# Optimization experiments

Hardware: AMD Instinct MI355X
Metric: run time of the kernel (lower is better)

The kernel has to match this reference:

```python
import jax, jax.numpy as jnp
import numpy as np


def setup_inputs() -> dict:
    key = jax.random.key(0)
    k1, k2, k3 = jax.random.split(key, 3)
    B, K, NPC, D = 64, 1000, 256, 768
    querys = jax.random.normal(k1, (B, D), dtype=jnp.float32)
    data = jax.random.normal(k2, (K, NPC, D), dtype=jnp.float32)      # clustered doc embeddings
    centers = jax.random.normal(k3, (K, D), dtype=jnp.float32)        # cluster centroids
    clusted_idx = jnp.arange(K * NPC, dtype=jnp.int32).reshape(K, NPC)  # global doc id per slot
    return {
        'querys': querys,
        'data': data,
        'centers': centers,
        'clusted_idx': clusted_idx,
        'k': 16,
        'num_search': 10,
    }


def reference(querys, data, centers, clusted_idx, k, num_search):
    """Clustered (IVF-style) cosine top-k search.
    querys: (B,D); data: (K,NPC,D); centers: (K,D); clusted_idx: (K,NPC)
    returns ret_idx (B,k) int, ret_emb (B,k,D) float.
    dist_fn = -cos_sim, so argmin dist == argmax cosine.
    """
    B, D = querys.shape
    eps = jnp.float32(1e-12)
    qn = querys / jnp.maximum(jnp.linalg.norm(querys, axis=1, keepdims=True), eps)
    cn = centers / jnp.maximum(jnp.linalg.norm(centers, axis=1, keepdims=True), eps)

    # ---- first(): pick num_search closest clusters by cosine ----
    cos_c = qn @ cn.T                              # (B, K)
    _, c_idx = jax.lax.top_k(cos_c, num_search)    # (B, S) smallest -cos == largest cos

    # ---- second(): exact cosine search inside selected clusters ----
    cand = data[c_idx]                             # (B, S, NPC, D) gather
    cand_ids = clusted_idx[c_idx]                  # (B, S, NPC)
    cand_norm = jnp.maximum(jnp.linalg.norm(cand, axis=-1), eps)  # (B, S, NPC)
    cos = jnp.einsum('bd,bsnd->bsn', qn, cand) / cand_norm        # (B, S, NPC)

    # ---- merge: global top-k over all candidates ----
    cos_flat = cos.reshape(B, -1)                  # (B, S*NPC)
    _, top = jax.lax.top_k(cos_flat, k)            # (B, k)
    ret_idx = jnp.take_along_axis(cand_ids.reshape(B, -1), top, axis=1)            # (B, k)
    ret_emb = jnp.take_along_axis(cand.reshape(B, -1, D), top[..., None], axis=1)  # (B, k, D)
    return ret_idx, ret_emb
```

## Files before the change

kernel.cpp:

```cpp
#include <hip/hip_runtime.h>
#include <math.h>

#define BQ   64
#define KC   1000
#define NPC  256
#define DIM  768
#define TOPK 16
#define NS   10

#define NEG_INF (-__builtin_inff())

#define DOT12(acc, A, Bv) \
    acc = fmaf(A.x, Bv.x, acc); acc = fmaf(A.y, Bv.y, acc); \
    acc = fmaf(A.z, Bv.z, acc); acc = fmaf(A.w, Bv.w, acc);

__global__ void knorm_q(const float* __restrict__ q, float* __restrict__ qn,
                        int* __restrict__ cnt) {
    int b = blockIdx.x, t = threadIdx.x;
    if (b < 4 && t < 250) cnt[b * 250 + t] = 0;
    const float* row = q + b * DIM;
    float v0 = row[t], v1 = row[t + 256], v2 = row[t + 512];
    __shared__ float red[256];
    red[t] = v0 * v0 + v1 * v1 + v2 * v2;
    __syncthreads();
    for (int off = 128; off; off >>= 1) {
        if (t < off) red[t] += red[t + off];
        __syncthreads();
    }
    float scale = 1.0f / fmaxf(sqrtf(red[0]), 1e-12f);
    qn[b * DIM + t]       = v0 * scale;
    qn[b * DIM + t + 256] = v1 * scale;
    qn[b * DIM + t + 512] = v2 * scale;
}

__global__ void kcenter_scores(const float* __restrict__ qn,
                               const float* __restrict__ centers,
                               float* __restrict__ cosc) {
    int wave = threadIdx.x >> 6, lane = threadIdx.x & 63;
    int cblk = blockIdx.x >> 2, qg = blockIdx.x & 3;
    int k0 = cblk * 4 + wave;
    const float4* cp = (const float4*)(centers + (size_t)k0 * DIM);
    float4 c0 = cp[lane], c1 = cp[lane + 64], c2 = cp[lane + 128];
    float sq = 0.f;
    DOT12(sq, c0, c0); DOT12(sq, c1, c1); DOT12(sq, c2, c2);
    for (int off = 1; off < 64; off <<= 1) sq += __shfl_xor(sq, off);
    float inv = 1.0f / fmaxf(sqrtf(sq), 1e-12f);
    int b0 = qg * 16;
    for (int i = 0; i < 16; i += 4) {
        const float4* qa = (const float4*)(qn + (size_t)(b0 + i + 0) * DIM);
        const float4* qb = (const float4*)(qn + (size_t)(b0 + i + 1) * DIM);
        const float4* qc = (const float4*)(qn + (size_t)(b0 + i + 2) * DIM);
        const float4* qd = (const float4*)(qn + (size_t)(b0 + i + 3) * DIM);
        float4 a0 = qa[lane], a1 = qa[lane + 64], a2 = qa[lane + 128];
        float4 e0 = qb[lane], e1 = qb[lane + 64], e2 = qb[lane + 128];
        float4 f0 = qc[lane], f1 = qc[lane + 64], f2 = qc[lane + 128];
        float4 g0 = qd[lane], g1 = qd[lane + 64], g2 = qd[lane + 128];
        float dA = 0.f, dB = 0.f, dC = 0.f, dD = 0.f;
        DOT12(dA, a0, c0); DOT12(dA, a1, c1); DOT12(dA, a2, c2);
        DOT12(dB, e0, c0); DOT12(dB, e1, c1); DOT12(dB, e2, c2);
        DOT12(dC, f0, c0); DOT12(dC, f1, c1); DOT12(dC, f2, c2);
        DOT12(dD, g0, c0); DOT12(dD, g1, c1); DOT12(dD, g2, c2);
        for (int off = 1; off < 64; off <<= 1) {
            dA += __shfl_xor(dA, off);
            dB += __shfl_xor(dB, off);
            dC += __shfl_xor(dC, off);
            dD += __shfl_xor(dD, off);
        }
        if (lane == 0) {
            cosc[(b0 + i + 0) * KC + k0] = dA * inv;
            cosc[(b0 + i + 1) * KC + k0] = dB * inv;
            cosc[(b0 + i + 2) * KC + k0] = dC * inv;
            cosc[(b0 + i + 3) * KC + k0] = dD * inv;
        }
    }
}

__device__ __forceinline__ void wave_argmax(float& bv, int& bi) {
    for (int off = 1; off < 64; off <<= 1) {
        float v2 = __shfl_xor(bv, off);
        int   i2 = __shfl_xor(bi, off);
        if (v2 > bv || (v2 == bv && i2 < bi)) { bv = v2; bi = i2; }
    }
}

__global__ void ktop_clusters(const float* __restrict__ cosc, int* __restrict__ cidx,
                              int* __restrict__ cnt, int* __restrict__ sel) {
    int b = blockIdx.x, t = threadIdx.x;
    int wave = t >> 6, lane = t & 63;
    __shared__ float vals[KC];
    __shared__ float wrv[4];
    __shared__ int   wri[4];
    for (int i = t; i < KC; i += 256) vals[i] = cosc[b * KC + i];
    __syncthreads();
    for (int s = 0; s < NS; ++s) {
        float bv = NEG_INF; int bi = 0x7fffffff;
        for (int i = t; i < KC; i += 256) {
            float v = vals[i];
            if (v > bv) { bv = v; bi = i; }
        }
        wave_argmax(bv, bi);
        if (lane == 0) { wrv[wave] = bv; wri[wave] = bi; }
        __syncthreads();
        if (t == 0) {
            float fv = wrv[0]; int fi = wri[0];
            for (int w = 1; w < 4; ++w) {
                float v2 = wrv[w]; int i2 = wri[w];
                if (v2 > fv || (v2 == fv && i2 < fi)) { fv = v2; fi = i2; }
            }
            cidx[b * NS + s] = fi;
            int pos = atomicAdd(&cnt[fi], 1);
            sel[fi * 64 + pos] = b * NS + s;
            vals[fi] = NEG_INF;
        }
        __syncthreads();
    }
}

__global__ void kcand(const float* __restrict__ qn, const float* __restrict__ data,
                      const int* __restrict__ cnt, const int* __restrict__ sel,
                      float* __restrict__ cosall) {
    int c = blockIdx.x >> 2, sub = blockIdx.x & 3;
    int m = cnt[c];
    if (m == 0) return;
    int t = threadIdx.x;
    __shared__ int slist[64];
    if (t < m) slist[t] = sel[c * 64 + t];
    __syncthreads();
    int wave = t >> 6, lane = t & 63;
    const float* base = data + (size_t)c * NPC * DIM;
    int n0 = sub * 64 + wave * 16;
    for (int it = 0; it < 4; ++it) {
        int n = n0 + it * 4;
        const float4* dpa = (const float4*)(base + (size_t)(n + 0) * DIM);
        const float4* dpb = (const float4*)(base + (size_t)(n + 1) * DIM);
        const float4* dpc = (const float4*)(base + (size_t)(n + 2) * DIM);
        const float4* dpd = (const float4*)(base + (size_t)(n + 3) * DIM);
        float4 a0 = dpa[lane], a1 = dpa[lane + 64], a2 = dpa[lane + 128];
        float4 e0 = dpb[lane], e1 = dpb[lane + 64], e2 = dpb[lane + 128];
        float4 f0 = dpc[lane], f1 = dpc[lane + 64], f2 = dpc[lane + 128];
        float4 g0 = dpd[lane], g1 = dpd[lane + 64], g2 = dpd[lane + 128];
        float sqA = 0.f, sqB = 0.f, sqC = 0.f, sqD = 0.f;
        DOT12(sqA, a0, a0); DOT12(sqA, a1, a1); DOT12(sqA, a2, a2);
        DOT12(sqB, e0, e0); DOT12(sqB, e1, e1); DOT12(sqB, e2, e2);
        DOT12(sqC, f0, f0); DOT12(sqC, f1, f1); DOT12(sqC, f2, f2);
        DOT12(sqD, g0, g0); DOT12(sqD, g1, g1); DOT12(sqD, g2, g2);
        for (int off = 1; off < 64; off <<= 1) {
            sqA += __shfl_xor(sqA, off); sqB += __shfl_xor(sqB, off);
            sqC += __shfl_xor(sqC, off); sqD += __shfl_xor(sqD, off);
        }
        float invA = 1.0f / fmaxf(sqrtf(sqA), 1e-12f);
        float invB = 1.0f / fmaxf(sqrtf(sqB), 1e-12f);
        float invC = 1.0f / fmaxf(sqrtf(sqC), 1e-12f);
        float invD = 1.0f / fmaxf(sqrtf(sqD), 1e-12f);
        for (int j = 0; j < m; ++j) {
            int i = slist[j];
            int b = i / NS;
            const float4* qp = (const float4*)(qn + (size_t)b * DIM);
            float4 q0 = qp[lane], q1 = qp[lane + 64], q2 = qp[lane + 128];
            float dA = 0.f, dB = 0.f, dC = 0.f, dD = 0.f;
            DOT12(dA, q0, a0); DOT12(dA, q1, a1); DOT12(dA, q2, a2);
            DOT12(dB, q0, e0); DOT12(dB, q1, e1); DOT12(dB, q2, e2);
            DOT12(dC, q0, f0); DOT12(dC, q1, f1); DOT12(dC, q2, f2);
            DOT12(dD, q0, g0); DOT12(dD, q1, g1); DOT12(dD, q2, g2);
            for (int off = 1; off < 64; off <<= 1) {
                dA += __shfl_xor(dA, off); dB += __shfl_xor(dB, off);
                dC += __shfl_xor(dC, off); dD += __shfl_xor(dD, off);
            }
            if (lane == 0) {
                float* outp = cosall + (size_t)i * NPC + n;
                outp[0] = dA * invA;
                outp[1] = dB * invB;
                outp[2] = dC * invC;
                outp[3] = dD * invD;
            }
        }
    }
}

__global__ void ktop_final(const float* __restrict__ cosall, const int* __restrict__ cidx,
                           const int* __restrict__ clusted, const float* __restrict__ data,
                           float* __restrict__ out) {
    int b = blockIdx.x, t = threadIdx.x;
    int wave = t >> 6, lane = t & 63;
    __shared__ float vals[NS * NPC];
    __shared__ float wrv[4];
    __shared__ int   wri[4];
    __shared__ int   docs[TOPK];
    for (int i = t; i < NS * NPC; i += 256) vals[i] = cosall[(size_t)b * (NS * NPC) + i];
    __syncthreads();
    for (int j = 0; j < TOPK; ++j) {
        float bv = NEG_INF; int bi = 0x7fffffff;
        for (int i = t; i < NS * NPC; i += 256) {
            float v = vals[i];
            if (v > bv) { bv = v; bi = i; }
        }
        wave_argmax(bv, bi);
        if (lane == 0) { wrv[wave] = bv; wri[wave] = bi; }
        __syncthreads();
        if (t == 0) {
            float fv = wrv[0]; int fi = wri[0];
            for (int w = 1; w < 4; ++w) {
                float v2 = wrv[w]; int i2 = wri[w];
                if (v2 > fv || (v2 == fv && i2 < fi)) { fv = v2; fi = i2; }
            }
            int s = fi >> 8, n = fi & (NPC - 1);
            int c = cidx[b * NS + s];
            int doc = c * NPC + n;
            docs[j] = doc;
            out[b * TOPK + j] = (float)clusted[doc];
            vals[fi] = NEG_INF;
        }
        __syncthreads();
    }
    float* emb = out + BQ * TOPK;
    for (int idx = t; idx < TOPK * (DIM / 4); idx += 256) {
        int j = idx / (DIM / 4), col = idx - j * (DIM / 4);
        int doc = docs[j];
        ((float4*)(emb + ((size_t)(b * TOPK + j)) * DIM))[col] =
            ((const float4*)(data + (size_t)doc * DIM))[col];
    }
}

extern "C" void kernel_launch(void* const* d_in, const int* in_sizes, int n_in,
                              void* d_out, int out_size, void* d_ws, size_t ws_size,
                              hipStream_t stream) {
    const float* querys  = (const float*)d_in[0];
    const float* data    = (const float*)d_in[1];
    const float* centers = (const float*)d_in[2];
    const int*   clusted = (const int*)d_in[3];
    float* out = (float*)d_out;

    float* ws     = (float*)d_ws;
    float* qn     = ws;
    float* cosc   = qn + BQ * DIM;
    int*   cidx   = (int*)(cosc + BQ * KC);
    float* cosall = (float*)(cidx + BQ * NS);
    int*   cnt    = (int*)(cosall + BQ * NS * NPC);
    int*   sel    = cnt + KC;

    knorm_q<<<BQ, 256, 0, stream>>>(querys, qn, cnt);
    kcenter_scores<<<KC, 256, 0, stream>>>(qn, centers, cosc);
    ktop_clusters<<<BQ, 256, 0, stream>>>(cosc, cidx, cnt, sel);
    kcand<<<KC * 4, 256, 0, stream>>>(qn, data, cnt, sel, cosall);
    ktop_final<<<BQ, 256, 0, stream>>>(cosall, cidx, clusted, data, out);
}
```

Measured before the change: 143.1 us.

## Drop query normalization kernel and restage candidate scoring through LDS tiles

Removes the query-normalization kernel and feeds raw queries to the center and candidate scoring, since a positive per-query scale does not change the per-query top-k ranking. The counter reset moves into kcenter_scores. The candidate kernel now uses one block per cluster with one thread per document. Each block stages 32-wide D chunks of the cluster into padded LDS and accumulates up to 8 query dot products per thread, replacing the wave-per-doc shuffle reductions. This cuts launches and reduction overhead but lowers parallelism (1000 blocks instead of 4000) and reads query rows from global memory uncached in LDS. It also changes output cosine magnitudes, which is safe only if later stages compare values and never output them.

```diff
diff --git a/kernel.cpp b/kernel.cpp
--- a/kernel.cpp
+++ b/kernel.cpp
@@ -14,28 +14,12 @@
     acc = fmaf(A.x, Bv.x, acc); acc = fmaf(A.y, Bv.y, acc); \
     acc = fmaf(A.z, Bv.z, acc); acc = fmaf(A.w, Bv.w, acc);
 
-__global__ void knorm_q(const float* __restrict__ q, float* __restrict__ qn,
-                        int* __restrict__ cnt) {
-    int b = blockIdx.x, t = threadIdx.x;
-    if (b < 4 && t < 250) cnt[b * 250 + t] = 0;
-    const float* row = q + b * DIM;
-    float v0 = row[t], v1 = row[t + 256], v2 = row[t + 512];
-    __shared__ float red[256];
-    red[t] = v0 * v0 + v1 * v1 + v2 * v2;
-    __syncthreads();
-    for (int off = 128; off; off >>= 1) {
-        if (t < off) red[t] += red[t + off];
-        __syncthreads();
-    }
-    float scale = 1.0f / fmaxf(sqrtf(red[0]), 1e-12f);
-    qn[b * DIM + t]       = v0 * scale;
-    qn[b * DIM + t + 256] = v1 * scale;
-    qn[b * DIM + t + 512] = v2 * scale;
-}
-
-__global__ void kcenter_scores(const float* __restrict__ qn,
+
+__global__ void kcenter_scores(const float* __restrict__ q,
                                const float* __restrict__ centers,
-                               float* __restrict__ cosc) {
+                               float* __restrict__ cosc,
+                               int* __restrict__ cnt) {
+    if (threadIdx.x == 0) cnt[blockIdx.x] = 0;
     int wave = threadIdx.x >> 6, lane = threadIdx.x & 63;
     int cblk = blockIdx.x >> 2, qg = blockIdx.x & 3;
     int k0 = cblk * 4 + wave;
@@ -47,10 +31,10 @@
     float inv = 1.0f / fmaxf(sqrtf(sq), 1e-12f);
     int b0 = qg * 16;
     for (int i = 0; i < 16; i += 4) {
-        const float4* qa = (const float4*)(qn + (size_t)(b0 + i + 0) * DIM);
-        const float4* qb = (const float4*)(qn + (size_t)(b0 + i + 1) * DIM);
-        const float4* qc = (const float4*)(qn + (size_t)(b0 + i + 2) * DIM);
-        const float4* qd = (const float4*)(qn + (size_t)(b0 + i + 3) * DIM);
+        const float4* qa = (const float4*)(q + (size_t)(b0 + i + 0) * DIM);
+        const float4* qb = (const float4*)(q + (size_t)(b0 + i + 1) * DIM);
+        const float4* qc = (const float4*)(q + (size_t)(b0 + i + 2) * DIM);
+        const float4* qd = (const float4*)(q + (size_t)(b0 + i + 3) * DIM);
         float4 a0 = qa[lane], a1 = qa[lane + 64], a2 = qa[lane + 128];
         float4 e0 = qb[lane], e1 = qb[lane + 64], e2 = qb[lane + 128];
         float4 f0 = qc[lane], f1 = qc[lane + 64], f2 = qc[lane + 128];
@@ -116,64 +100,78 @@
     }
 }
 
-__global__ void kcand(const float* __restrict__ qn, const float* __restrict__ data,
-                      const int* __restrict__ cnt, const int* __restrict__ sel,
-                      float* __restrict__ cosall) {
-    int c = blockIdx.x >> 2, sub = blockIdx.x & 3;
+#define CH    32
+#define NCH   (DIM / CH)
+#define STR   36
+#define MAXM  8
+
+__global__ __launch_bounds__(256) void kcand(const float* __restrict__ q,
+                                             const float* __restrict__ data,
+                                             const int* __restrict__ cnt,
+                                             const int* __restrict__ sel,
+                                             float* __restrict__ cosall) {
+    int c = blockIdx.x;
     int m = cnt[c];
     if (m == 0) return;
     int t = threadIdx.x;
+    __shared__ float lds[NPC * STR];
     __shared__ int slist[64];
     if (t < m) slist[t] = sel[c * 64 + t];
+    const float4* dbase = (const float4*)data + (size_t)c * NPC * (DIM / 4);
+    const float4* q4    = (const float4*)q;
     __syncthreads();
-    int wave = t >> 6, lane = t & 63;
-    const float* base = data + (size_t)c * NPC * DIM;
-    int n0 = sub * 64 + wave * 16;
-    for (int it = 0; it < 4; ++it) {
-        int n = n0 + it * 4;
-        const float4* dpa = (const float4*)(base + (size_t)(n + 0) * DIM);
-        const float4* dpb = (const float4*)(base + (size_t)(n + 1) * DIM);
-        const float4* dpc = (const float4*)(base + (size_t)(n + 2) * DIM);
-        const float4* dpd = (const float4*)(base + (size_t)(n + 3) * DIM);
-        float4 a0 = dpa[lane], a1 = dpa[lane + 64], a2 = dpa[lane + 128];
-        float4 e0 = dpb[lane], e1 = dpb[lane + 64], e2 = dpb[lane + 128];
-        float4 f0 = dpc[lane], f1 = dpc[lane + 64], f2 = dpc[lane + 128];
-        float4 g0 = dpd[lane], g1 = dpd[lane + 64], g2 = dpd[lane + 128];
-        float sqA = 0.f, sqB = 0.f, sqC = 0.f, sqD = 0.f;
-        DOT12(sqA, a0, a0); DOT12(sqA, a1, a1); DOT12(sqA, a2, a2);
-        DOT12(sqB, e0, e0); DOT12(sqB, e1, e1); DOT12(sqB, e2, e2);
-        DOT12(sqC, f0, f0); DOT12(sqC, f1, f1); DOT12(sqC, f2, f2);
-        DOT12(sqD, g0, g0); DOT12(sqD, g1, g1); DOT12(sqD, g2, g2);
-        for (int off = 1; off < 64; off <<= 1) {
-            sqA += __shfl_xor(sqA, off); sqB += __shfl_xor(sqB, off);
-            sqC += __shfl_xor(sqC, off); sqD += __shfl_xor(sqD, off);
-        }
-        float invA = 1.0f / fmaxf(sqrtf(sqA), 1e-12f);
-        float invB = 1.0f / fmaxf(sqrtf(sqB), 1e-12f);
-        float invC = 1.0f / fmaxf(sqrtf(sqC), 1e-12f);
-        float invD = 1.0f / fmaxf(sqrtf(sqD), 1e-12f);
-        for (int j = 0; j < m; ++j) {
-            int i = slist[j];
-            int b = i / NS;
-            const float4* qp = (const float4*)(qn + (size_t)b * DIM);
-            float4 q0 = qp[lane], q1 = qp[lane + 64], q2 = qp[lane + 128];
-            float dA = 0.f, dB = 0.f, dC = 0.f, dD = 0.f;
-            DOT12(dA, q0, a0); DOT12(dA, q1, a1); DOT12(dA, q2, a2);
-            DOT12(dB, q0, e0); DOT12(dB, q1, e1); DOT12(dB, q2, e2);
-            DOT12(dC, q0, f0); DOT12(dC, q1, f1); DOT12(dC, q2, f2);
-            DOT12(dD, q0, g0); DOT12(dD, q1, g1); DOT12(dD, q2, g2);
-            for (int off = 1; off < 64; off <<= 1) {
-                dA += __shfl_xor(dA, off); dB += __shfl_xor(dB, off);
-                dC += __shfl_xor(dC, off); dD += __shfl_xor(dD, off);
-            }
-            if (lane == 0) {
-                float* outp = cosall + (size_t)i * NPC + n;
-                outp[0] = dA * invA;
-                outp[1] = dB * invB;
-                outp[2] = dC * invC;
-                outp[3] = dD * invD;
-            }
-        }
+
+    for (int j0 = 0; j0 < m; j0 += MAXM) {
+        int mm = min(m - j0, MAXM);
+        int qrow[MAXM];
+#pragma unroll
+        for (int jj = 0; jj < MAXM; ++jj) {
+            int si = slist[(jj < mm) ? (j0 + jj) : j0];
+            qrow[jj] = __builtin_amdgcn_readfirstlane(si / NS);
+        }
+        float acc[MAXM];
+#pragma unroll
+        for (int jj = 0; jj < MAXM; ++jj) acc[jj] = 0.f;
+        float sq = 0.f;
+
+        for (int k = 0; k < NCH; ++k) {
+            __syncthreads();
+#pragma unroll
+            for (int i = 0; i < 8; ++i) {
+                int F = i * 256 + t;
+                int d = F >> 3, s = F & 7;
+                float4 v = dbase[(size_t)d * (DIM / 4) + k * 8 + s];
+                *(float4*)&lds[d * STR + s * 4] = v;
+            }
+            __syncthreads();
+            float4 dv[8];
+#pragma unroll
+            for (int s = 0; s < 8; ++s) dv[s] = *(const float4*)&lds[t * STR + s * 4];
+#pragma unroll
+            for (int s = 0; s < 8; ++s) { DOT12(sq, dv[s], dv[s]); }
+#pragma unroll
+            for (int jj = 0; jj < MAXM; ++jj) {
+                if (jj < mm) {
+                    const float4* qp = q4 + (size_t)qrow[jj] * (DIM / 4) + k * 8;
+                    float a = acc[jj];
+#pragma unroll
+                    for (int s = 0; s < 8; ++s) {
+                        float4 qv = qp[s];
+                        DOT12(a, dv[s], qv);
+                    }
+                    acc[jj] = a;
+                }
+            }
+        }
+        float invd = 1.0f / fmaxf(sqrtf(sq), 1e-12f);
+#pragma unroll
+        for (int jj = 0; jj < MAXM; ++jj) {
+            if (jj < mm) {
+                int i = slist[j0 + jj];
+                cosall[(size_t)i * NPC + t] = acc[jj] * invd;
+            }
+        }
+        __syncthreads();
     }
 }
 
@@ -231,16 +229,14 @@
     float* out = (float*)d_out;
 
     float* ws     = (float*)d_ws;
-    float* qn     = ws;
-    float* cosc   = qn + BQ * DIM;
+    float* cosc   = ws;
     int*   cidx   = (int*)(cosc + BQ * KC);
     float* cosall = (float*)(cidx + BQ * NS);
     int*   cnt    = (int*)(cosall + BQ * NS * NPC);
     int*   sel    = cnt + KC;
 
-    knorm_q<<<BQ, 256, 0, stream>>>(querys, qn, cnt);
-    kcenter_scores<<<KC, 256, 0, stream>>>(qn, centers, cosc);
+    kcenter_scores<<<KC, 256, 0, stream>>>(querys, centers, cosc, cnt);
     ktop_clusters<<<BQ, 256, 0, stream>>>(cosc, cidx, cnt, sel);
-    kcand<<<KC * 4, 256, 0, stream>>>(qn, data, cnt, sel, cosall);
+    kcand<<<KC, 256, 0, stream>>>(querys, data, cnt, sel, cosall);
     ktop_final<<<BQ, 256, 0, stream>>>(cosall, cidx, clusted, data, out);
 }
```

After: 167.1 us. +16.8%, slower.
